# Optimization experiments

Hardware: AMD Instinct MI355X
Metric: run time of the kernel (lower is better)

The kernel has to match this reference:

```python
import jax, jax.numpy as jnp
import numpy as np

TOP_K = 2

def setup_inputs() -> dict:
    key = jax.random.key(0)
    ks = jax.random.split(key, 6)
    B, S, D, H, E = 2, 1024, 512, 1024, 8
    x = jax.random.normal(ks[0], (B, S, D), dtype=jnp.float32)
    w_router = jax.random.normal(ks[1], (E, D), dtype=jnp.float32) / np.sqrt(D)
    b_router = jnp.zeros((E,), dtype=jnp.float32)
    w1 = jax.random.normal(ks[2], (E, H, D), dtype=jnp.float32) / np.sqrt(D)   # per-expert fc1 (hidden, in)
    w2 = jax.random.normal(ks[3], (E, D, H), dtype=jnp.float32) / np.sqrt(H)   # per-expert fc2 (out, hidden)
    return {"x": x, "w_router": w_router, "b_router": b_router, "w1": w1, "w2": w2}


def reference(x, w_router, b_router, w1, w2):
    B, S, D = x.shape
    E = w_router.shape[0]
    x_flat = x.reshape(-1, D)                                  # [T, D]
    # Router: logits -> softmax -> top-k -> renormalize -> dispatch weights
    router_logits = x_flat @ w_router.T + b_router             # [T, E]
    probs = jax.nn.softmax(router_logits, axis=-1)
    top_p, top_i = jax.lax.top_k(probs, TOP_K)                 # [T, K]
    top_p = top_p / jnp.sum(top_p, axis=-1, keepdims=True)
    # dispatch[t, e] = normalized prob if e in top-k of t else 0
    dispatch = jnp.sum(jax.nn.one_hot(top_i, E, dtype=x.dtype) * top_p[..., None], axis=1)  # [T, E]
    # Dense-masked expert MLP (mathematically identical to gather/GEMM/scatter):
    h = jax.nn.gelu(jnp.einsum('td,ehd->teh', x_flat, w1), approximate=False)  # [T, E, H]
    y = jnp.einsum('teh,edh->ted', h, w2)                      # [T, E, Dout]
    out = jnp.einsum('ted,te->td', y, dispatch)                # weighted combine
    out = out.reshape(B, S, -1)
    return out, router_logits
```

## Files before the change

### kernel.cpp

```cpp
#include <hip/hip_runtime.h>
#include <hip/hip_bf16.h>
#include <math.h>

#define T_TOK 2048
#define DIM 512
#define HID 1024
#define NE 8
#define CAP 1024

#define ROUT_BLKS 128
#define CAST_BLKS 2048

typedef __attribute__((ext_vector_type(8))) short short8;
typedef __attribute__((ext_vector_type(4))) float floatx4;

__device__ __forceinline__ unsigned short f2bf_bits(float f) {
    __hip_bfloat16 h = __float2bfloat16(f);
    return *reinterpret_cast<unsigned short*>(&h);
}

__device__ __forceinline__ void gl2lds(const unsigned short* g, unsigned short* l) {
    __builtin_amdgcn_global_load_lds(
        (const __attribute__((address_space(1))) unsigned int*)g,
        (__attribute__((address_space(3))) unsigned int*)l, 16, 0, 0);
}

__device__ __forceinline__ short8 frag(const unsigned short* s, int row, int kg) {
    return *reinterpret_cast<const short8*>(s + row * 128 + (((kg) ^ (row & 7)) << 3));
}

template<int T>
__device__ __forceinline__ void stage_tile(const unsigned short* src, size_t RS,
                                           int k0, unsigned short* lds,
                                           int wave, int lane) {
    int ro = lane >> 4, gr = lane & 15;
#pragma unroll
    for (int i = wave; i < T / 4; i += 4) {
        int r = i * 4 + ro;
        gl2lds(src + (size_t)r * RS + k0 + (((gr ^ (r & 7)) << 3)),
               lds + i * 512);
    }
}

__global__ __launch_bounds__(256)
void prep(const float* __restrict__ x, const float* __restrict__ wr,
          const float* __restrict__ br,
          const float* __restrict__ w1, const float* __restrict__ w2,
          unsigned short* __restrict__ w1b, unsigned short* __restrict__ w2b,
          unsigned short* __restrict__ xg, int* __restrict__ counts,
          int2* __restrict__ pairSlot, float2* __restrict__ pw,
          float* __restrict__ logits_out) {
    int bx = blockIdx.x;
    int tid = threadIdx.x;
    if (bx >= ROUT_BLKS) {
        const int n1 = NE * HID * DIM / 4;
        int base = (bx - ROUT_BLKS) * 1024 + tid;
#pragma unroll
        for (int rep = 0; rep < 4; rep++) {
            int i = base + rep * 256;
            const float* s = (i < n1) ? w1 : w2;
            unsigned short* d = (i < n1) ? w1b : w2b;
            int j = (i < n1) ? i : i - n1;
            float4 v = reinterpret_cast<const float4*>(s)[j];
            ushort4 o;
            o.x = f2bf_bits(v.x); o.y = f2bf_bits(v.y);
            o.z = f2bf_bits(v.z); o.w = f2bf_bits(v.w);
            reinterpret_cast<ushort4*>(d)[j] = o;
        }
        return;
    }
    int wave = tid >> 6, lane = tid & 63;
    for (int it = 0; it < 4; it++) {
        int t = bx * 16 + it * 4 + wave;
        const float4* xr = reinterpret_cast<const float4*>(x + (size_t)t * DIM);
        float4 xa = xr[lane * 2], xc = xr[lane * 2 + 1];
        short8 o;
        o[0] = (short)f2bf_bits(xa.x); o[1] = (short)f2bf_bits(xa.y);
        o[2] = (short)f2bf_bits(xa.z); o[3] = (short)f2bf_bits(xa.w);
        o[4] = (short)f2bf_bits(xc.x); o[5] = (short)f2bf_bits(xc.y);
        o[6] = (short)f2bf_bits(xc.z); o[7] = (short)f2bf_bits(xc.w);
        float p[NE];
#pragma unroll
        for (int e = 0; e < NE; e++) {
            const float4* wre = reinterpret_cast<const float4*>(wr + e * DIM);
            float4 wa = wre[lane * 2], wc = wre[lane * 2 + 1];
            p[e] = xa.x * wa.x + xa.y * wa.y + xa.z * wa.z + xa.w * wa.w
                 + xc.x * wc.x + xc.y * wc.y + xc.z * wc.z + xc.w * wc.w;
        }
#pragma unroll
        for (int e = 0; e < NE; e++) {
#pragma unroll
            for (int off = 32; off >= 1; off >>= 1)
                p[e] += __shfl_xor(p[e], off, 64);
        }
        int slot1 = 0, slot2 = 0;
        if (lane == 0) {
            float l[NE];
#pragma unroll
            for (int e = 0; e < NE; e++) {
                l[e] = p[e] + br[e];
                logits_out[(size_t)t * NE + e] = l[e];
            }
            int e1 = 0;
#pragma unroll
            for (int e = 1; e < NE; e++) if (l[e] > l[e1]) e1 = e;
            int es = -1;
#pragma unroll
            for (int e = 0; e < NE; e++) {
                if (e == e1) continue;
                if (es < 0 || l[e] > l[es]) es = e;
            }
            float z = expf(l[es] - l[e1]);
            float inv = 1.f / (1.f + z);
            int pos1 = atomicAdd(&counts[e1 * 16], 1);
            if (pos1 > CAP - 1) pos1 = CAP - 1;
            int pos2 = atomicAdd(&counts[es * 16], 1);
            if (pos2 > CAP - 1) pos2 = CAP - 1;
            slot1 = e1 * CAP + pos1;
            slot2 = es * CAP + pos2;
            pairSlot[t] = make_int2(slot1, slot2);
            pw[t] = make_float2(inv, z * inv);
        }
        slot1 = __shfl(slot1, 0);
        slot2 = __shfl(slot2, 0);
        *reinterpret_cast<short8*>(xg + (size_t)slot1 * DIM + lane * 8) = o;
        *reinterpret_cast<short8*>(xg + (size_t)slot2 * DIM + lane * 8) = o;
    }
}

__global__ __launch_bounds__(256, 3)
void gemm1(const unsigned short* __restrict__ xg,
           const unsigned short* __restrict__ w1b,
           const int* __restrict__ counts,
           unsigned short* __restrict__ Hb) {
    int bx = blockIdx.x;
    int e = bx & 7;
    int rest = bx >> 3;
    int n0 = (rest & 7) * 128;
    int m0 = (rest >> 3) * 64;
    int cnt = counts[e * 16]; if (cnt > CAP) cnt = CAP;
    if (m0 >= cnt) return;

    __shared__ __align__(16) unsigned short s_a[64 * 128];
    __shared__ __align__(16) unsigned short s_b[128 * 128];

    int tid = threadIdx.x, wave = tid >> 6, lane = tid & 63;
    int g = lane >> 4, ln = lane & 15;
    int wm = wave & 1, wn = wave >> 1;

    const unsigned short* asrc = xg + (size_t)(e * CAP + m0) * DIM;
    const unsigned short* bsrc = w1b + (size_t)(e * HID + n0) * DIM;

    floatx4 acc[2][4];
#pragma unroll
    for (int mf = 0; mf < 2; mf++)
#pragma unroll
        for (int nf = 0; nf < 4; nf++) acc[mf][nf] = (floatx4){0.f, 0.f, 0.f, 0.f};

    for (int ph = 0; ph < 4; ph++) {
        int k0 = ph * 128;
        stage_tile<64>(asrc, DIM, k0, s_a, wave, lane);
        stage_tile<128>(bsrc, DIM, k0, s_b, wave, lane);
        __syncthreads();
#pragma unroll
        for (int ks = 0; ks < 4; ks++) {
            short8 a0 = frag(s_a, wm * 32 + ln, ks * 4 + g);
            short8 a1 = frag(s_a, wm * 32 + 16 + ln, ks * 4 + g);
#pragma unroll
            for (int nf = 0; nf < 4; nf++) {
                short8 b = frag(s_b, wn * 64 + nf * 16 + ln, ks * 4 + g);
                acc[0][nf] = __builtin_amdgcn_mfma_f32_16x16x32_bf16(a0, b, acc[0][nf], 0, 0, 0);
                acc[1][nf] = __builtin_amdgcn_mfma_f32_16x16x32_bf16(a1, b, acc[1][nf], 0, 0, 0);
            }
        }
        __syncthreads();
    }
#pragma unroll
    for (int mf = 0; mf < 2; mf++)
#pragma unroll
        for (int nf = 0; nf < 4; nf++)
#pragma unroll
            for (int r = 0; r < 4; r++) {
                int lr = wm * 32 + mf * 16 + g * 4 + r;
                int col = n0 + wn * 64 + nf * 16 + ln;
                float v = acc[mf][nf][r];
                float gv = 0.5f * v * (1.f + erff(v * 0.70710678118f));
                Hb[(size_t)(e * CAP + m0 + lr) * HID + col] = f2bf_bits(gv);
            }
}

__global__ __launch_bounds__(256, 3)
void gemm2(const unsigned short* __restrict__ Hb,
           const unsigned short* __restrict__ w2b,
           const int* __restrict__ counts,
           float* __restrict__ ybuf) {
    int bx = blockIdx.x;
    int e = bx & 7;
    int rest = bx >> 3;
    int n0 = (rest & 3) * 128;
    int kv = (rest >> 2) & 1;
    int m0 = (rest >> 3) * 64;
    int cnt = counts[e * 16]; if (cnt > CAP) cnt = CAP;
    if (m0 >= cnt) return;

    __shared__ __align__(16) unsigned short s_a[64 * 128];
    __shared__ __align__(16) unsigned short s_b[128 * 128];

    int tid = threadIdx.x, wave = tid >> 6, lane = tid & 63;
    int g = lane >> 4, ln = lane & 15;
    int wm = wave & 1, wn = wave >> 1;

    const unsigned short* asrc = Hb + (size_t)(e * CAP + m0) * HID;
    const unsigned short* bsrc = w2b + (size_t)(e * DIM + n0) * HID;

    floatx4 acc[2][4];
#pragma unroll
    for (int mf = 0; mf < 2; mf++)
#pragma unroll
        for (int nf = 0; nf < 4; nf++) acc[mf][nf] = (floatx4){0.f, 0.f, 0.f, 0.f};

    for (int ph = 0; ph < 4; ph++) {
        int k0 = kv * 512 + ph * 128;
        stage_tile<64>(asrc, HID, k0, s_a, wave, lane);
        stage_tile<128>(bsrc, HID, k0, s_b, wave, lane);
        __syncthreads();
#pragma unroll
        for (int ks = 0; ks < 4; ks++) {
            short8 a0 = frag(s_a, wm * 32 + ln, ks * 4 + g);
            short8 a1 = frag(s_a, wm * 32 + 16 + ln, ks * 4 + g);
#pragma unroll
            for (int nf = 0; nf < 4; nf++) {
                short8 b = frag(s_b, wn * 64 + nf * 16 + ln, ks * 4 + g);
                acc[0][nf] = __builtin_amdgcn_mfma_f32_16x16x32_bf16(a0, b, acc[0][nf], 0, 0, 0);
                acc[1][nf] = __builtin_amdgcn_mfma_f32_16x16x32_bf16(a1, b, acc[1][nf], 0, 0, 0);
            }
        }
        __syncthreads();
    }
    float* yb = ybuf + (size_t)kv * (NE * CAP * DIM);
#pragma unroll
    for (int mf = 0; mf < 2; mf++)
#pragma unroll
        for (int nf = 0; nf < 4; nf++)
#pragma unroll
            for (int r = 0; r < 4; r++) {
                int lr = wm * 32 + mf * 16 + g * 4 + r;
                int col = n0 + wn * 64 + nf * 16 + ln;
                yb[(size_t)(e * CAP + m0 + lr) * DIM + col] = acc[mf][nf][r];
            }
}

__global__ __launch_bounds__(256)
void combine_kernel(const float* __restrict__ ybuf, const int2* __restrict__ pairSlot,
                    const float2* __restrict__ pw, float* __restrict__ out) {
    int id = blockIdx.x * 256 + threadIdx.x;
    int t = id >> 7, dv = id & 127;
    int2 s = pairSlot[t];
    float2 w = pw[t];
    const size_t KV = (size_t)NE * CAP * DIM;
    const float4* y0a = reinterpret_cast<const float4*>(ybuf + (size_t)s.x * DIM);
    const float4* y1a = reinterpret_cast<const float4*>(ybuf + KV + (size_t)s.x * DIM);
    const float4* y0b = reinterpret_cast<const float4*>(ybuf + (size_t)s.y * DIM);
    const float4* y1b = reinterpret_cast<const float4*>(ybuf + KV + (size_t)s.y * DIM);
    float4 a = y0a[dv], b = y1a[dv], c = y0b[dv], d = y1b[dv];
    float4 r;
    r.x = w.x * (a.x + b.x) + w.y * (c.x + d.x);
    r.y = w.x * (a.y + b.y) + w.y * (c.y + d.y);
    r.z = w.x * (a.z + b.z) + w.y * (c.z + d.z);
    r.w = w.x * (a.w + b.w) + w.y * (c.w + d.w);
    reinterpret_cast<float4*>(out)[(size_t)t * 128 + dv] = r;
}

extern "C" void kernel_launch(void* const* d_in, const int* in_sizes, int n_in,
                              void* d_out, int out_size, void* d_ws, size_t ws_size,
                              hipStream_t stream) {
    const float* x  = (const float*)d_in[0];
    const float* wr = (const float*)d_in[1];
    const float* br = (const float*)d_in[2];
    const float* w1 = (const float*)d_in[3];
    const float* w2 = (const float*)d_in[4];
    float* out = (float*)d_out;
    float* logits_out = out + (size_t)T_TOK * DIM;

    char* ws = (char*)d_ws;
    int*    counts   = (int*)ws;
    int2*   pairSlot = (int2*)(ws + 4096);
    float2* pw       = (float2*)(ws + 24576);
    unsigned short* xg  = (unsigned short*)(ws + 131072);
    unsigned short* w1b = (unsigned short*)(ws + 8519680);
    unsigned short* w2b = (unsigned short*)(ws + 16908288);
    unsigned short* Hb  = (unsigned short*)(ws + 25296896);
    float*          ybuf = (float*)(ws + 42074112);

    hipMemsetAsync(counts, 0, 512, stream);

    prep<<<ROUT_BLKS + CAST_BLKS, 256, 0, stream>>>(
        x, wr, br, w1, w2, w1b, w2b, xg, counts, pairSlot, pw, logits_out);

    gemm1<<<NE * 16 * 8, 256, 0, stream>>>(xg, w1b, counts, Hb);

    gemm2<<<NE * 16 * 2 * 4, 256, 0, stream>>>(Hb, w2b, counts, ybuf);

    combine_kernel<<<1024, 256, 0, stream>>>(ybuf, pairSlot, pw, out);
}
```

Baseline: 126.2 us.

## Fuse weight bf16 cast into GEMM staging and combine into gemm2 via atomics

```diff
diff --git a/kernel.cpp b/kernel.cpp
--- a/kernel.cpp
+++ b/kernel.cpp
@@ -9,7 +9,7 @@
 #define CAP 1024
 
 #define ROUT_BLKS 128
-#define CAST_BLKS 2048
+#define ZERO_BLKS 256
 
 typedef __attribute__((ext_vector_type(8))) short short8;
 typedef __attribute__((ext_vector_type(4))) float floatx4;
@@ -42,31 +42,38 @@
     }
 }
 
+template<int R>
+__device__ __forceinline__ void stage_f32(const float* src, size_t RS, int k0,
+                                          unsigned short* lds, int tid) {
+    int gr = tid & 15, r0 = tid >> 4;
+#pragma unroll 4
+    for (int i = 0; i < R / 16; i++) {
+        int r = r0 + i * 16;
+        const float4* s = reinterpret_cast<const float4*>(src + (size_t)r * RS + k0 + gr * 8);
+        float4 va = s[0], vb = s[1];
+        short8 o;
+        o[0] = (short)f2bf_bits(va.x); o[1] = (short)f2bf_bits(va.y);
+        o[2] = (short)f2bf_bits(va.z); o[3] = (short)f2bf_bits(va.w);
+        o[4] = (short)f2bf_bits(vb.x); o[5] = (short)f2bf_bits(vb.y);
+        o[6] = (short)f2bf_bits(vb.z); o[7] = (short)f2bf_bits(vb.w);
+        *reinterpret_cast<short8*>(lds + r * 128 + ((gr ^ (r & 7)) << 3)) = o;
+    }
+}
+
 __global__ __launch_bounds__(256)
 void prep(const float* __restrict__ x, const float* __restrict__ wr,
           const float* __restrict__ br,
-          const float* __restrict__ w1, const float* __restrict__ w2,
-          unsigned short* __restrict__ w1b, unsigned short* __restrict__ w2b,
           unsigned short* __restrict__ xg, int* __restrict__ counts,
-          int2* __restrict__ pairSlot, float2* __restrict__ pw,
-          float* __restrict__ logits_out) {
+          int* __restrict__ tokOf, float* __restrict__ wOf,
+          float* __restrict__ out, float* __restrict__ logits_out) {
     int bx = blockIdx.x;
     int tid = threadIdx.x;
     if (bx >= ROUT_BLKS) {
-        const int n1 = NE * HID * DIM / 4;
-        int base = (bx - ROUT_BLKS) * 1024 + tid;
-#pragma unroll
-        for (int rep = 0; rep < 4; rep++) {
-            int i = base + rep * 256;
-            const float* s = (i < n1) ? w1 : w2;
-            unsigned short* d = (i < n1) ? w1b : w2b;
-            int j = (i < n1) ? i : i - n1;
-            float4 v = reinterpret_cast<const float4*>(s)[j];
-            ushort4 o;
-            o.x = f2bf_bits(v.x); o.y = f2bf_bits(v.y);
-            o.z = f2bf_bits(v.z); o.w = f2bf_bits(v.w);
-            reinterpret_cast<ushort4*>(d)[j] = o;
-        }
+        float4 z; z.x = z.y = z.z = z.w = 0.f;
+        int base = (bx - ROUT_BLKS) * 256 + tid;
+#pragma unroll
+        for (int rep = 0; rep < 4; rep++)
+            reinterpret_cast<float4*>(out)[base + rep * 65536] = z;
         return;
     }
     int wave = tid >> 6, lane = tid & 63;
@@ -118,8 +125,8 @@
             if (pos2 > CAP - 1) pos2 = CAP - 1;
             slot1 = e1 * CAP + pos1;
             slot2 = es * CAP + pos2;
-            pairSlot[t] = make_int2(slot1, slot2);
-            pw[t] = make_float2(inv, z * inv);
+            tokOf[slot1] = t; wOf[slot1] = inv;
+            tokOf[slot2] = t; wOf[slot2] = z * inv;
         }
         slot1 = __shfl(slot1, 0);
         slot2 = __shfl(slot2, 0);
@@ -130,7 +137,7 @@
 
 __global__ __launch_bounds__(256, 3)
 void gemm1(const unsigned short* __restrict__ xg,
-           const unsigned short* __restrict__ w1b,
+           const float* __restrict__ w1,
            const int* __restrict__ counts,
            unsigned short* __restrict__ Hb) {
     int bx = blockIdx.x;
@@ -149,7 +156,7 @@
     int wm = wave & 1, wn = wave >> 1;
 
     const unsigned short* asrc = xg + (size_t)(e * CAP + m0) * DIM;
-    const unsigned short* bsrc = w1b + (size_t)(e * HID + n0) * DIM;
+    const float* bsrc = w1 + (size_t)(e * HID + n0) * DIM;
 
     floatx4 acc[2][4];
 #pragma unroll
@@ -160,7 +167,7 @@
     for (int ph = 0; ph < 4; ph++) {
         int k0 = ph * 128;
         stage_tile<64>(asrc, DIM, k0, s_a, wave, lane);
-        stage_tile<128>(bsrc, DIM, k0, s_b, wave, lane);
+        stage_f32<128>(bsrc, DIM, k0, s_b, tid);
         __syncthreads();
 #pragma unroll
         for (int ks = 0; ks < 4; ks++) {
@@ -191,9 +198,10 @@
 
 __global__ __launch_bounds__(256, 3)
 void gemm2(const unsigned short* __restrict__ Hb,
-           const unsigned short* __restrict__ w2b,
+           const float* __restrict__ w2,
            const int* __restrict__ counts,
-           float* __restrict__ ybuf) {
+           const int* __restrict__ tokOf, const float* __restrict__ wOf,
+           float* __restrict__ out) {
     int bx = blockIdx.x;
     int e = bx & 7;
     int rest = bx >> 3;
@@ -211,7 +219,7 @@
     int wm = wave & 1, wn = wave >> 1;
 
     const unsigned short* asrc = Hb + (size_t)(e * CAP + m0) * HID;
-    const unsigned short* bsrc = w2b + (size_t)(e * DIM + n0) * HID;
+    const float* bsrc = w2 + (size_t)(e * DIM + n0) * HID;
 
     floatx4 acc[2][4];
 #pragma unroll
@@ -222,7 +230,7 @@
     for (int ph = 0; ph < 4; ph++) {
         int k0 = kv * 512 + ph * 128;
         stage_tile<64>(asrc, HID, k0, s_a, wave, lane);
-        stage_tile<128>(bsrc, HID, k0, s_b, wave, lane);
+        stage_f32<128>(bsrc, HID, k0, s_b, tid);
         __syncthreads();
 #pragma unroll
         for (int ks = 0; ks < 4; ks++) {
@@ -237,38 +245,21 @@
         }
         __syncthreads();
     }
-    float* yb = ybuf + (size_t)kv * (NE * CAP * DIM);
-#pragma unroll
-    for (int mf = 0; mf < 2; mf++)
-#pragma unroll
-        for (int nf = 0; nf < 4; nf++)
-#pragma unroll
-            for (int r = 0; r < 4; r++) {
-                int lr = wm * 32 + mf * 16 + g * 4 + r;
-                int col = n0 + wn * 64 + nf * 16 + ln;
-                yb[(size_t)(e * CAP + m0 + lr) * DIM + col] = acc[mf][nf][r];
-            }
-}
-
-__global__ __launch_bounds__(256)
-void combine_kernel(const float* __restrict__ ybuf, const int2* __restrict__ pairSlot,
-                    const float2* __restrict__ pw, float* __restrict__ out) {
-    int id = blockIdx.x * 256 + threadIdx.x;
-    int t = id >> 7, dv = id & 127;
-    int2 s = pairSlot[t];
-    float2 w = pw[t];
-    const size_t KV = (size_t)NE * CAP * DIM;
-    const float4* y0a = reinterpret_cast<const float4*>(ybuf + (size_t)s.x * DIM);
-    const float4* y1a = reinterpret_cast<const float4*>(ybuf + KV + (size_t)s.x * DIM);
-    const float4* y0b = reinterpret_cast<const float4*>(ybuf + (size_t)s.y * DIM);
-    const float4* y1b = reinterpret_cast<const float4*>(ybuf + KV + (size_t)s.y * DIM);
-    float4 a = y0a[dv], b = y1a[dv], c = y0b[dv], d = y1b[dv];
-    float4 r;
-    r.x = w.x * (a.x + b.x) + w.y * (c.x + d.x);
-    r.y = w.x * (a.y + b.y) + w.y * (c.y + d.y);
-    r.z = w.x * (a.z + b.z) + w.y * (c.z + d.z);
-    r.w = w.x * (a.w + b.w) + w.y * (c.w + d.w);
-    reinterpret_cast<float4*>(out)[(size_t)t * 128 + dv] = r;
+#pragma unroll
+    for (int mf = 0; mf < 2; mf++)
+#pragma unroll
+        for (int r = 0; r < 4; r++) {
+            int lr = wm * 32 + mf * 16 + g * 4 + r;
+            int row = m0 + lr;
+            if (row >= cnt) continue;
+            int slot = e * CAP + row;
+            int t = tokOf[slot];
+            float w = wOf[slot];
+            float* orow = out + (size_t)t * DIM + n0 + wn * 64 + ln;
+#pragma unroll
+            for (int nf = 0; nf < 4; nf++)
+                atomicAdd(orow + nf * 16, w * acc[mf][nf][r]);
+        }
 }
 
 extern "C" void kernel_launch(void* const* d_in, const int* in_sizes, int n_in,
@@ -283,23 +274,18 @@
     float* logits_out = out + (size_t)T_TOK * DIM;
 
     char* ws = (char*)d_ws;
-    int*    counts   = (int*)ws;
-    int2*   pairSlot = (int2*)(ws + 4096);
-    float2* pw       = (float2*)(ws + 24576);
-    unsigned short* xg  = (unsigned short*)(ws + 131072);
-    unsigned short* w1b = (unsigned short*)(ws + 8519680);
-    unsigned short* w2b = (unsigned short*)(ws + 16908288);
-    unsigned short* Hb  = (unsigned short*)(ws + 25296896);
-    float*          ybuf = (float*)(ws + 42074112);
+    int*   counts = (int*)ws;
+    int*   tokOf  = (int*)(ws + 4096);
+    float* wOf    = (float*)(ws + 40960);
+    unsigned short* xg = (unsigned short*)(ws + 131072);
+    unsigned short* Hb = (unsigned short*)(ws + 8519680);
 
     hipMemsetAsync(counts, 0, 512, stream);
 
-    prep<<<ROUT_BLKS + CAST_BLKS, 256, 0, stream>>>(
-        x, wr, br, w1, w2, w1b, w2b, xg, counts, pairSlot, pw, logits_out);
-
-    gemm1<<<NE * 16 * 8, 256, 0, stream>>>(xg, w1b, counts, Hb);
-
-    gemm2<<<NE * 16 * 2 * 4, 256, 0, stream>>>(Hb, w2b, counts, ybuf);
-
-    combine_kernel<<<1024, 256, 0, stream>>>(ybuf, pairSlot, pw, out);
-}
+    prep<<<ROUT_BLKS + ZERO_BLKS, 256, 0, stream>>>(
+        x, wr, br, xg, counts, tokOf, wOf, out, logits_out);
+
+    gemm1<<<NE * 16 * 8, 256, 0, stream>>>(xg, w1, counts, Hb);
+
+    gemm2<<<NE * 16 * 2 * 4, 256, 0, stream>>>(Hb, w2, counts, tokOf, wOf, out);
+}
```

After: 138.7 us. +9.9%, slower.

## Fuse weighted combine into gemm2 epilogue via atomic adds to output

Applied to the files above, without the earlier changes.

```diff
diff --git a/kernel.cpp b/kernel.cpp
--- a/kernel.cpp
+++ b/kernel.cpp
@@ -10,6 +10,7 @@
 
 #define ROUT_BLKS 128
 #define CAST_BLKS 2048
+#define ZERO_BLKS 256
 
 typedef __attribute__((ext_vector_type(8))) short short8;
 typedef __attribute__((ext_vector_type(4))) float floatx4;
@@ -48,10 +49,18 @@
           const float* __restrict__ w1, const float* __restrict__ w2,
           unsigned short* __restrict__ w1b, unsigned short* __restrict__ w2b,
           unsigned short* __restrict__ xg, int* __restrict__ counts,
-          int2* __restrict__ pairSlot, float2* __restrict__ pw,
-          float* __restrict__ logits_out) {
+          int* __restrict__ tokOf, float* __restrict__ wOf,
+          float* __restrict__ out, float* __restrict__ logits_out) {
     int bx = blockIdx.x;
     int tid = threadIdx.x;
+    if (bx >= ROUT_BLKS + CAST_BLKS) {
+        float4 z; z.x = z.y = z.z = z.w = 0.f;
+        int base = (bx - ROUT_BLKS - CAST_BLKS) * 1024 + tid;
+#pragma unroll
+        for (int rep = 0; rep < 4; rep++)
+            reinterpret_cast<float4*>(out)[base + rep * 256] = z;
+        return;
+    }
     if (bx >= ROUT_BLKS) {
         const int n1 = NE * HID * DIM / 4;
         int base = (bx - ROUT_BLKS) * 1024 + tid;
@@ -118,8 +127,8 @@
             if (pos2 > CAP - 1) pos2 = CAP - 1;
             slot1 = e1 * CAP + pos1;
             slot2 = es * CAP + pos2;
-            pairSlot[t] = make_int2(slot1, slot2);
-            pw[t] = make_float2(inv, z * inv);
+            tokOf[slot1] = t; wOf[slot1] = inv;
+            tokOf[slot2] = t; wOf[slot2] = z * inv;
         }
         slot1 = __shfl(slot1, 0);
         slot2 = __shfl(slot2, 0);
@@ -193,7 +202,8 @@
 void gemm2(const unsigned short* __restrict__ Hb,
            const unsigned short* __restrict__ w2b,
            const int* __restrict__ counts,
-           float* __restrict__ ybuf) {
+           const int* __restrict__ tokOf, const float* __restrict__ wOf,
+           float* __restrict__ out) {
     int bx = blockIdx.x;
     int e = bx & 7;
     int rest = bx >> 3;
@@ -237,38 +247,21 @@
         }
         __syncthreads();
     }
-    float* yb = ybuf + (size_t)kv * (NE * CAP * DIM);
-#pragma unroll
-    for (int mf = 0; mf < 2; mf++)
-#pragma unroll
-        for (int nf = 0; nf < 4; nf++)
-#pragma unroll
-            for (int r = 0; r < 4; r++) {
-                int lr = wm * 32 + mf * 16 + g * 4 + r;
-                int col = n0 + wn * 64 + nf * 16 + ln;
-                yb[(size_t)(e * CAP + m0 + lr) * DIM + col] = acc[mf][nf][r];
-            }
-}
-
-__global__ __launch_bounds__(256)
-void combine_kernel(const float* __restrict__ ybuf, const int2* __restrict__ pairSlot,
-                    const float2* __restrict__ pw, float* __restrict__ out) {
-    int id = blockIdx.x * 256 + threadIdx.x;
-    int t = id >> 7, dv = id & 127;
-    int2 s = pairSlot[t];
-    float2 w = pw[t];
-    const size_t KV = (size_t)NE * CAP * DIM;
-    const float4* y0a = reinterpret_cast<const float4*>(ybuf + (size_t)s.x * DIM);
-    const float4* y1a = reinterpret_cast<const float4*>(ybuf + KV + (size_t)s.x * DIM);
-    const float4* y0b = reinterpret_cast<const float4*>(ybuf + (size_t)s.y * DIM);
-    const float4* y1b = reinterpret_cast<const float4*>(ybuf + KV + (size_t)s.y * DIM);
-    float4 a = y0a[dv], b = y1a[dv], c = y0b[dv], d = y1b[dv];
-    float4 r;
-    r.x = w.x * (a.x + b.x) + w.y * (c.x + d.x);
-    r.y = w.x * (a.y + b.y) + w.y * (c.y + d.y);
-    r.z = w.x * (a.z + b.z) + w.y * (c.z + d.z);
-    r.w = w.x * (a.w + b.w) + w.y * (c.w + d.w);
-    reinterpret_cast<float4*>(out)[(size_t)t * 128 + dv] = r;
+#pragma unroll
+    for (int mf = 0; mf < 2; mf++)
+#pragma unroll
+        for (int r = 0; r < 4; r++) {
+            int lr = wm * 32 + mf * 16 + g * 4 + r;
+            int row = m0 + lr;
+            if (row >= cnt) continue;
+            int slot = e * CAP + row;
+            int t = tokOf[slot];
+            float w = wOf[slot];
+            float* orow = out + (size_t)t * DIM + n0 + wn * 64 + ln;
+#pragma unroll
+            for (int nf = 0; nf < 4; nf++)
+                atomicAdd(orow + nf * 16, w * acc[mf][nf][r]);
+        }
 }
 
 extern "C" void kernel_launch(void* const* d_in, const int* in_sizes, int n_in,
@@ -283,23 +276,20 @@
     float* logits_out = out + (size_t)T_TOK * DIM;
 
     char* ws = (char*)d_ws;
-    int*    counts   = (int*)ws;
-    int2*   pairSlot = (int2*)(ws + 4096);
-    float2* pw       = (float2*)(ws + 24576);
+    int*   counts = (int*)ws;
+    int*   tokOf  = (int*)(ws + 4096);
+    float* wOf    = (float*)(ws + 40960);
     unsigned short* xg  = (unsigned short*)(ws + 131072);
     unsigned short* w1b = (unsigned short*)(ws + 8519680);
     unsigned short* w2b = (unsigned short*)(ws + 16908288);
     unsigned short* Hb  = (unsigned short*)(ws + 25296896);
-    float*          ybuf = (float*)(ws + 42074112);
 
     hipMemsetAsync(counts, 0, 512, stream);
 
-    prep<<<ROUT_BLKS + CAST_BLKS, 256, 0, stream>>>(
-        x, wr, br, w1, w2, w1b, w2b, xg, counts, pairSlot, pw, logits_out);
+    prep<<<ROUT_BLKS + CAST_BLKS + ZERO_BLKS, 256, 0, stream>>>(
+        x, wr, br, w1, w2, w1b, w2b, xg, counts, tokOf, wOf, out, logits_out);
 
     gemm1<<<NE * 16 * 8, 256, 0, stream>>>(xg, w1b, counts, Hb);
 
-    gemm2<<<NE * 16 * 2 * 4, 256, 0, stream>>>(Hb, w2b, counts, ybuf);
-
-    combine_kernel<<<1024, 256, 0, stream>>>(ybuf, pairSlot, pw, out);
-}
+    gemm2<<<NE * 16 * 2 * 4, 256, 0, stream>>>(Hb, w2b, counts, tokOf, wOf, out);
+}
```

Result: slower. 133.0 us (+5.3%).

## Move w2 bf16 cast from prep kernel into gemm1 launch to overlap

Applied to the files above, without the earlier changes.

```diff
diff --git a/kernel.cpp b/kernel.cpp
--- a/kernel.cpp
+++ b/kernel.cpp
@@ -9,7 +9,9 @@
 #define CAP 1024
 
 #define ROUT_BLKS 128
-#define CAST_BLKS 2048
+#define CAST1_BLKS 1024
+#define GEMM1_BLKS (NE * 16 * 8)
+#define CAST2_BLKS 256
 
 typedef __attribute__((ext_vector_type(8))) short short8;
 typedef __attribute__((ext_vector_type(4))) float floatx4;
@@ -45,27 +47,23 @@
 __global__ __launch_bounds__(256)
 void prep(const float* __restrict__ x, const float* __restrict__ wr,
           const float* __restrict__ br,
-          const float* __restrict__ w1, const float* __restrict__ w2,
-          unsigned short* __restrict__ w1b, unsigned short* __restrict__ w2b,
+          const float* __restrict__ w1,
+          unsigned short* __restrict__ w1b,
           unsigned short* __restrict__ xg, int* __restrict__ counts,
           int2* __restrict__ pairSlot, float2* __restrict__ pw,
           float* __restrict__ logits_out) {
     int bx = blockIdx.x;
     int tid = threadIdx.x;
     if (bx >= ROUT_BLKS) {
-        const int n1 = NE * HID * DIM / 4;
         int base = (bx - ROUT_BLKS) * 1024 + tid;
 #pragma unroll
         for (int rep = 0; rep < 4; rep++) {
-            int i = base + rep * 256;
-            const float* s = (i < n1) ? w1 : w2;
-            unsigned short* d = (i < n1) ? w1b : w2b;
-            int j = (i < n1) ? i : i - n1;
-            float4 v = reinterpret_cast<const float4*>(s)[j];
+            int j = base + rep * 256;
+            float4 v = reinterpret_cast<const float4*>(w1)[j];
             ushort4 o;
             o.x = f2bf_bits(v.x); o.y = f2bf_bits(v.y);
             o.z = f2bf_bits(v.z); o.w = f2bf_bits(v.w);
-            reinterpret_cast<ushort4*>(d)[j] = o;
+            reinterpret_cast<ushort4*>(w1b)[j] = o;
         }
         return;
     }
@@ -132,8 +130,24 @@
 void gemm1(const unsigned short* __restrict__ xg,
            const unsigned short* __restrict__ w1b,
            const int* __restrict__ counts,
-           unsigned short* __restrict__ Hb) {
+           unsigned short* __restrict__ Hb,
+           const float* __restrict__ w2,
+           unsigned short* __restrict__ w2b) {
     int bx = blockIdx.x;
+    int tid = threadIdx.x;
+    if (bx >= GEMM1_BLKS) {
+        int base = (bx - GEMM1_BLKS) * 4096 + tid;
+#pragma unroll
+        for (int rep = 0; rep < 16; rep++) {
+            int j = base + rep * 256;
+            float4 v = reinterpret_cast<const float4*>(w2)[j];
+            ushort4 o;
+            o.x = f2bf_bits(v.x); o.y = f2bf_bits(v.y);
+            o.z = f2bf_bits(v.z); o.w = f2bf_bits(v.w);
+            reinterpret_cast<ushort4*>(w2b)[j] = o;
+        }
+        return;
+    }
     int e = bx & 7;
     int rest = bx >> 3;
     int n0 = (rest & 7) * 128;
@@ -144,7 +158,7 @@
     __shared__ __align__(16) unsigned short s_a[64 * 128];
     __shared__ __align__(16) unsigned short s_b[128 * 128];
 
-    int tid = threadIdx.x, wave = tid >> 6, lane = tid & 63;
+    int wave = tid >> 6, lane = tid & 63;
     int g = lane >> 4, ln = lane & 15;
     int wm = wave & 1, wn = wave >> 1;
 
@@ -294,10 +308,11 @@
 
     hipMemsetAsync(counts, 0, 512, stream);
 
-    prep<<<ROUT_BLKS + CAST_BLKS, 256, 0, stream>>>(
-        x, wr, br, w1, w2, w1b, w2b, xg, counts, pairSlot, pw, logits_out);
-
-    gemm1<<<NE * 16 * 8, 256, 0, stream>>>(xg, w1b, counts, Hb);
+    prep<<<ROUT_BLKS + CAST1_BLKS, 256, 0, stream>>>(
+        x, wr, br, w1, w1b, xg, counts, pairSlot, pw, logits_out);
+
+    gemm1<<<GEMM1_BLKS + CAST2_BLKS, 256, 0, stream>>>(
+        xg, w1b, counts, Hb, w2, w2b);
 
     gemm2<<<NE * 16 * 2 * 4, 256, 0, stream>>>(Hb, w2b, counts, ybuf);
 
```

New measurement: 127.6 us. No clear change (+1.1%).
